# Kernel optimization log

Hardware: AMD Instinct MI355X
Metric: run time of the kernel (lower is better)

The kernel has to match this reference:

```python
import jax, jax.numpy as jnp
import numpy as np

T, B, N, H, NT = 4096, 8, 256, 512, 5
W_SCALE = 0.02


def setup_inputs() -> dict:
    key = jax.random.key(0)
    ks = jax.random.split(key, 32)
    f32 = jnp.float32
    d = {}
    d['v_action'] = jax.random.normal(ks[0], (N, B, H), f32)
    d['v_frame'] = jax.random.normal(ks[1], (T, B, H), f32)
    d['v_task'] = jax.random.normal(ks[2], (NT, B, H), f32)
    d['v_mask'] = jax.random.randint(ks[3], (B, N), 0, 2, jnp.int32).at[:, 0].set(1)
    d['t_action'] = jax.random.normal(ks[4], (N, B, H), f32)
    d['t_frame'] = jax.random.normal(ks[5], (T, B, H), f32)
    d['t_task'] = jax.random.normal(ks[6], (NT, B, H), f32)
    d['t_mask'] = jax.random.randint(ks[7], (B, N), 0, 2, jnp.int32).at[:, 0].set(1)
    names = ['v_Wq', 'v_Wk', 'v_Wv', 'v_Wo', 't_Wq', 't_Wk', 't_Wv', 't_Wo']
    for i, nm in enumerate(names):
        d[nm] = jax.random.normal(ks[8 + i], (H, H), f32) * W_SCALE
    d['v_aw'] = jnp.asarray(0.1, f32)
    d['t_aw'] = jnp.asarray(0.1, f32)
    d['v_tw'] = jax.random.normal(ks[20], (H, 1), f32) * W_SCALE
    d['v_tb'] = jnp.zeros((1,), f32)
    d['t_tw'] = jax.random.normal(ks[21], (H, 1), f32) * W_SCALE
    d['t_tb'] = jnp.zeros((1,), f32)
    return d


def _compute_logit(frame, action, Wq, Wk):
    # frame: [T,B,H] queries, action: [N,B,H] keys -> logits [B,T,N]
    q = jnp.einsum('tbf,fh->tbh', frame, Wq)
    k = jnp.einsum('nba,ah->nbh', action, Wk)
    return jnp.einsum('tbh,nbh->btn', q, k) / jnp.sqrt(jnp.asarray(q.shape[-1], q.dtype))


def _compute_output(logit, alignment, action, frame, mask, Wv, Wo, aw):
    # shared detached cross-domain alignment, gated by sigmoid(alignment_weight)
    combined = logit + jax.nn.sigmoid(aw) * alignment          # [B,T,N]
    nomask = combined
    masked = jnp.where(mask[:, None, :] > 0, combined, -jnp.inf)
    attn = jax.nn.softmax(masked, axis=-1)                      # softmax over protos N
    v = jnp.einsum('nba,af->nbf', action, Wv)                   # values from protos
    out = jnp.einsum('btn,nbf->tbf', attn, v)
    out = jnp.einsum('tbf,fg->tbg', out, Wo) + frame            # residual to frames
    return out, nomask


def reference(v_action, v_frame, v_task, v_mask, t_action, t_frame, t_task, t_mask,
              v_Wq, v_Wk, v_Wv, v_Wo, v_aw, v_tw, v_tb,
              t_Wq, t_Wk, t_Wv, t_Wo, t_aw, t_tw, t_tb):
    v_logit = _compute_logit(v_frame, v_action, v_Wq, v_Wk)
    t_logit = _compute_logit(t_frame, t_action, t_Wq, t_Wk)
    v_share = jax.lax.stop_gradient(v_logit)
    t_share = jax.lax.stop_gradient(t_logit)
    v_out, v_nm = _compute_output(v_logit, t_share, v_action, v_frame, v_mask, v_Wv, v_Wo, v_aw)
    t_out, t_nm = _compute_output(t_logit, v_share, t_action, t_frame, t_mask, t_Wv, t_Wo, t_aw)
    v_ta = jnp.einsum('kbh,ho->kbo', v_task, v_tw) + v_tb       # [ntask,B,1]
    t_ta = jnp.einsum('kbh,ho->kbo', t_task, t_tw) + t_tb
    return (v_out, t_out,
            jnp.transpose(v_nm, (0, 2, 1)),                      # [B,N,T]
            jnp.transpose(t_nm, (0, 2, 1)),
            v_ta, t_ta)
```

## Files before the change

kernel.cpp:

```cpp
#include <hip/hip_runtime.h>
#include <hip/hip_bf16.h>
#include <cstddef>
#include <cstdint>

#define T_DIM 4096
#define B_DIM 8
#define N_DIM 256
#define H_DIM 512
#define NT_DIM 5

typedef __attribute__((ext_vector_type(8))) short short8;
typedef __attribute__((ext_vector_type(4))) float f32x4;

__device__ __forceinline__ short cvt_bf16(float f) {
  __hip_bfloat16 h = __float2bfloat16(f);
  union { __hip_bfloat16 h; short s; } u; u.h = h; return u.s;
}
__device__ __forceinline__ float bf2f(short s) {
  union { uint32_t u; float f; } v; v.u = ((uint32_t)(uint16_t)s) << 16;
  return v.f;
}

typedef __attribute__((address_space(1))) const void gvoid_t;
typedef __attribute__((address_space(3))) void lvoid_t;
__device__ __forceinline__ void gl_lds16(const void* g, void* lds_wave_base) {
  __builtin_amdgcn_global_load_lds((gvoid_t*)(uintptr_t)g,
                                   (lvoid_t*)(uint32_t)(uintptr_t)lds_wave_base,
                                   16, 0, 0);
}

#define MFMA16(a, b, c) __builtin_amdgcn_mfma_f32_16x16x32_bf16(a, b, c, 0, 0, 0)

struct GP {
  const void* A[2];
  const short* B[2];
  void* C[2];
  const float* R[2];
};

template<typename TA, typename TC, bool ADD_RES>
__global__ __launch_bounds__(256)
void gemm_tn(GP p, int zlog, long long a_bs, int lda,
             long long b_bs, int ldb, long long c_bs, int ldc,
             int K, float scale) {
  constexpr bool F32A = (sizeof(TA) == 4);
  constexpr int ASTR = F32A ? 40 : 32;
  constexpr int AB = 128 * ASTR * 2;
  constexpr int BB = 128 * 32 * 2;
  constexpr int HALF = AB + BB;
  constexpr int EPIB = 4 * 16 * 68 * 4;
  constexpr int BODYB = F32A ? (2 * AB + 3 * BB) : (3 * HALF);
  constexpr int SMEMB = BODYB > EPIB ? BODYB : EPIB;
  __shared__ __align__(16) char smem[SMEMB];

  const int tid  = threadIdx.x;
  const int lane = tid & 63;
  const int wave = tid >> 6;
  const int wr   = (wave >> 1) * 64;
  const int wc   = (wave & 1) * 64;
  const int lrow = lane & 15;
  const int kgrp = lane >> 4;

  const int dom = blockIdx.z >> zlog;
  const long long zz = blockIdx.z & ((1u << zlog) - 1u);

  const TA*    Abase = (const TA*)p.A[dom] + zz * a_bs + (long long)(blockIdx.x * 128) * lda;
  const short* Bbase = p.B[dom] + zz * b_bs + (long long)(blockIdx.y * 128) * ldb;

  const int ch_r  = lane >> 2;
  const int swcol = ((lane & 3) ^ (ch_r & 3)) * 8;
  const int srow = tid >> 1;
  const int scol = (tid & 1) * 16;

  f32x4 acc[4][4] = {};
  f32x4 pv[4];

  auto stageA_bf16 = [&](int buf, int k0) {
    short* As = (short*)(smem + buf * HALF);
    #pragma unroll
    for (int i = 0; i < 2; ++i) {
      const int c = wave + 4 * i;
      gl_lds16((const short*)Abase + (long long)(c * 16 + ch_r) * lda + k0 + swcol,
               &As[c * 512]);
    }
  };
  auto stageB_bf16 = [&](int buf, int k0) {
    short* Bs = (short*)(smem + buf * HALF + AB);
    #pragma unroll
    for (int i = 0; i < 2; ++i) {
      const int c = wave + 4 * i;
      gl_lds16(Bbase + (long long)(c * 16 + ch_r) * ldb + k0 + swcol, &Bs[c * 512]);
    }
  };
  auto stageB_f32p = [&](int buf, int k0) {
    short* Bs = (short*)(smem + 2 * AB + buf * BB);
    #pragma unroll
    for (int i = 0; i < 2; ++i) {
      const int c = wave + 4 * i;
      gl_lds16(Bbase + (long long)(c * 16 + ch_r) * ldb + k0 + swcol, &Bs[c * 512]);
    }
  };
  auto loadA_f32 = [&](int k0) {
    const float* gp = (const float*)Abase + (long long)srow * lda + k0 + scol;
    pv[0] = *(const f32x4*)(gp + 0);
    pv[1] = *(const f32x4*)(gp + 4);
    pv[2] = *(const f32x4*)(gp + 8);
    pv[3] = *(const f32x4*)(gp + 12);
  };
  auto writeA_f32 = [&](int buf) {
    short* As = (short*)(smem + buf * AB);
    short8 s0, s1;
    #pragma unroll
    for (int e = 0; e < 4; ++e) {
      s0[e]     = cvt_bf16(pv[0][e]);
      s0[4 + e] = cvt_bf16(pv[1][e]);
      s1[e]     = cvt_bf16(pv[2][e]);
      s1[4 + e] = cvt_bf16(pv[3][e]);
    }
    *(short8*)&As[srow * ASTR + scol]     = s0;
    *(short8*)&As[srow * ASTR + scol + 8] = s1;
  };
  auto compute = [&](int abuf, int bbuf) {
    const short* As = (const short*)(smem + (F32A ? abuf * AB : abuf * HALF));
    const short* Bs = (const short*)(smem + (F32A ? 2 * AB + bbuf * BB
                                                  : bbuf * HALF + AB));
    short8 af[4], bfr[4];
    const int u = kgrp ^ (lrow & 3);
    #pragma unroll
    for (int i = 0; i < 4; ++i) {
      const int row = wr + i * 16 + lrow;
      if constexpr (F32A) af[i] = *(const short8*)&As[row * ASTR + kgrp * 8];
      else                af[i] = *(const short8*)&As[row * 32 + u * 8];
    }
    #pragma unroll
    for (int j = 0; j < 4; ++j) {
      const int row = wc + j * 16 + lrow;
      bfr[j] = *(const short8*)&Bs[row * 32 + u * 8];
    }
    #pragma unroll
    for (int i = 0; i < 4; ++i)
      #pragma unroll
      for (int j = 0; j < 4; ++j)
        acc[i][j] = MFMA16(af[i], bfr[j], acc[i][j]);
  };

  const int NT = K >> 5;
  if constexpr (F32A) {
    loadA_f32(0); writeA_f32(0);
    stageB_f32p(0, 0);
    if (NT > 1) stageB_f32p(1, 32);
    if (NT > 1) loadA_f32(32);
    for (int t = 0; t < NT; ++t) {
      asm volatile("s_waitcnt lgkmcnt(0)" ::: "memory");
      __builtin_amdgcn_sched_barrier(0);
      __builtin_amdgcn_s_barrier();
      if (t + 2 < NT) stageB_f32p((t + 2) % 3, (t + 2) << 5);
      __builtin_amdgcn_sched_barrier(0);
      if (t + 2 < NT)      asm volatile("s_waitcnt vmcnt(8)" ::: "memory");
      else if (t + 1 < NT) asm volatile("s_waitcnt vmcnt(6)" ::: "memory");
      else                 asm volatile("s_waitcnt vmcnt(0)" ::: "memory");
      __builtin_amdgcn_sched_barrier(0);
      __builtin_amdgcn_s_barrier();
      __builtin_amdgcn_sched_barrier(0);
      compute(t & 1, t % 3);
      if (t + 1 < NT) writeA_f32((t + 1) & 1);
      if (t + 2 < NT) loadA_f32((t + 2) << 5);
    }
  } else {
    stageA_bf16(0, 0); stageB_bf16(0, 0);
    if (NT > 1) { stageA_bf16(1, 32); stageB_bf16(1, 32); }
    for (int t = 0; t < NT; ++t) {
      __builtin_amdgcn_s_barrier();
      if (t + 2 < NT) {
        stageA_bf16((t + 2) % 3, (t + 2) << 5);
        stageB_bf16((t + 2) % 3, (t + 2) << 5);
        __builtin_amdgcn_sched_barrier(0);
        asm volatile("s_waitcnt vmcnt(8)" ::: "memory");
      } else if (t + 1 < NT) {
        asm volatile("s_waitcnt vmcnt(4)" ::: "memory");
      } else {
        asm volatile("s_waitcnt vmcnt(0)" ::: "memory");
      }
      __builtin_amdgcn_sched_barrier(0);
      __builtin_amdgcn_s_barrier();
      __builtin_amdgcn_sched_barrier(0);
      compute(t % 3, t % 3);
    }
  }

  __syncthreads();
  float* myEp = (float*)smem + wave * (16 * 68);
  TC* Cd = (TC*)p.C[dom];
  const float* Res = p.R[dom];
  const long long cb = zz * c_bs;
  const int gm = blockIdx.x * 128 + wr;
  const int gn = blockIdx.y * 128 + wc;
  const int er = lane >> 2;
  const int ec = (lane & 3) * 16;

  f32x4 resA[4], resB[4];
  if constexpr (ADD_RES) {
    const long long b0 = cb + (long long)(gm + er) * ldc + gn + ec;
    #pragma unroll
    for (int q = 0; q < 4; ++q) resA[q] = *(const f32x4*)&Res[b0 + q * 4];
  }

  #pragma unroll
  for (int i = 0; i < 4; ++i) {
    if constexpr (ADD_RES) {
      if (i < 3) {
        const long long bn = cb + (long long)(gm + (i + 1) * 16 + er) * ldc + gn + ec;
        #pragma unroll
        for (int q = 0; q < 4; ++q) resB[q] = *(const f32x4*)&Res[bn + q * 4];
      }
    }
    #pragma unroll
    for (int j = 0; j < 4; ++j)
      #pragma unroll
      for (int r = 0; r < 4; ++r)
        myEp[(kgrp * 4 + r) * 68 + j * 16 + lrow] = acc[i][j][r];
    float vals[16];
    #pragma unroll
    for (int q = 0; q < 4; ++q) {
      f32x4 t4 = *(const f32x4*)&myEp[er * 68 + ec + q * 4];
      vals[q * 4 + 0] = t4[0]; vals[q * 4 + 1] = t4[1];
      vals[q * 4 + 2] = t4[2]; vals[q * 4 + 3] = t4[3];
    }
    const int row_g = gm + i * 16 + er;
    const long long base = cb + (long long)row_g * ldc + gn + ec;
    if constexpr (sizeof(TC) == 2) {
      short8 s0, s1;
      #pragma unroll
      for (int e = 0; e < 8; ++e) {
        s0[e] = cvt_bf16(vals[e] * scale);
        s1[e] = cvt_bf16(vals[8 + e] * scale);
      }
      *(short8*)&Cd[base]     = s0;
      *(short8*)&Cd[base + 8] = s1;
    } else {
      #pragma unroll
      for (int q = 0; q < 4; ++q) {
        f32x4 o;
        #pragma unroll
        for (int e = 0; e < 4; ++e) o[e] = vals[q * 4 + e] * scale;
        if constexpr (ADD_RES) {
          #pragma unroll
          for (int e = 0; e < 4; ++e) o[e] += resA[q][e];
        }
        *(f32x4*)&Cd[base + q * 4] = o;
      }
    }
    if constexpr (ADD_RES) {
      #pragma unroll
      for (int q = 0; q < 4; ++q) resA[q] = resB[q];
    }
  }
}

struct WSrc { const float* p[8]; };

__global__ __launch_bounds__(256)
void wtrans_kernel(WSrc s, short* __restrict__ dst) {
  __shared__ float tile[32][33];
  const int w = blockIdx.z;
  const float* src = s.p[w];
  short* d = dst + (long long)w * H_DIM * H_DIM;
  const int tx = threadIdx.x, ty = threadIdx.y;
  const int n0 = blockIdx.x * 32, k0 = blockIdx.y * 32;
  #pragma unroll
  for (int i = 0; i < 4; ++i)
    tile[ty + 8 * i][tx] = src[(long long)(k0 + ty + 8 * i) * H_DIM + n0 + tx];
  __syncthreads();
  #pragma unroll
  for (int i = 0; i < 4; ++i)
    d[(long long)(n0 + ty + 8 * i) * H_DIM + k0 + tx] = cvt_bf16(tile[tx][ty + 8 * i]);
}

__global__ __launch_bounds__(256)
void softmax_fused(const short* __restrict__ Lv, const short* __restrict__ Lt,
                   const int* __restrict__ vmask, const int* __restrict__ tmask,
                   const float* __restrict__ vaw, const float* __restrict__ taw,
                   short* __restrict__ Av, short* __restrict__ At,
                   float* __restrict__ Onm_v, float* __restrict__ Onm_t) {
  __shared__ float tile[16 * 260];
  __shared__ int msk[2][256];
  const int tid = threadIdx.x;
  const int b = blockIdx.y, t0 = blockIdx.x * 16;
  const int r = tid >> 4, seg = tid & 15;
  msk[0][tid] = vmask[b * 256 + tid];
  msk[1][tid] = tmask[b * 256 + tid];
  __syncthreads();
  const float sv = 1.f / (1.f + __expf(-vaw[0]));
  const float st = 1.f / (1.f + __expf(-taw[0]));
  const long long off = ((long long)b * T_DIM + t0 + r) * N_DIM + seg * 16;

  short8 lv0 = *(const short8*)&Lv[off];
  short8 lv1 = *(const short8*)&Lv[off + 8];
  short8 lt0 = *(const short8*)&Lt[off];
  short8 lt1 = *(const short8*)&Lt[off + 8];
  float cv[16], ct[16];
  #pragma unroll
  for (int i = 0; i < 8; ++i) {
    float a0 = bf2f(lv0[i]), b0 = bf2f(lt0[i]);
    float a1 = bf2f(lv1[i]), b1 = bf2f(lt1[i]);
    cv[i]     = a0 + sv * b0;  ct[i]     = b0 + st * a0;
    cv[8 + i] = a1 + sv * b1;  ct[8 + i] = b1 + st * a1;
  }

#define EMIT_DOMAIN(CVAL, DI, AOUT, ONM) do {                                   \
    const int4 mA = *(const int4*)&msk[DI][seg * 16 + 0];                       \
    const int4 mB = *(const int4*)&msk[DI][seg * 16 + 4];                       \
    const int4 mC = *(const int4*)&msk[DI][seg * 16 + 8];                       \
    const int4 mD = *(const int4*)&msk[DI][seg * 16 + 12];                      \
    const int mk[16] = {mA.x, mA.y, mA.z, mA.w, mB.x, mB.y, mB.z, mB.w,         \
                        mC.x, mC.y, mC.z, mC.w, mD.x, mD.y, mD.z, mD.w};        \
    float mx = -3.4e38f;                                                        \
    _Pragma("unroll")                                                           \
    for (int q = 0; q < 16; ++q) if (mk[q] > 0) mx = fmaxf(mx, CVAL[q]);        \
    _Pragma("unroll")                                                           \
    for (int sh = 1; sh < 16; sh <<= 1) mx = fmaxf(mx, __shfl_xor(mx, sh));     \
    float ev[16]; float ssum = 0.f;                                             \
    _Pragma("unroll")                                                           \
    for (int q = 0; q < 16; ++q) {                                              \
      ev[q] = (mk[q] > 0) ? __expf(CVAL[q] - mx) : 0.f; ssum += ev[q];          \
    }                                                                           \
    _Pragma("unroll")                                                           \
    for (int sh = 1; sh < 16; sh <<= 1) ssum += __shfl_xor(ssum, sh);           \
    const float inv = 1.f / ssum;                                               \
    short8 o0, o1;                                                              \
    _Pragma("unroll")                                                           \
    for (int q = 0; q < 8; ++q) {                                               \
      o0[q] = cvt_bf16(ev[q] * inv); o1[q] = cvt_bf16(ev[8 + q] * inv);         \
    }                                                                           \
    *(short8*)&AOUT[off] = o0; *(short8*)&AOUT[off + 8] = o1;                   \
    _Pragma("unroll")                                                           \
    for (int q = 0; q < 4; ++q) {                                               \
      f32x4 tv; tv[0] = CVAL[q * 4]; tv[1] = CVAL[q * 4 + 1];                   \
      tv[2] = CVAL[q * 4 + 2]; tv[3] = CVAL[q * 4 + 3];                         \
      *(f32x4*)&tile[r * 260 + seg * 16 + q * 4] = tv;                          \
    }                                                                           \
    __syncthreads();                                                            \
    {                                                                           \
      float* obase = &ONM[((long long)b * N_DIM + tid) * T_DIM + t0];           \
      _Pragma("unroll")                                                         \
      for (int g = 0; g < 4; ++g) {                                             \
        f32x4 wv;                                                               \
        wv[0] = tile[(4 * g + 0) * 260 + tid];                                  \
        wv[1] = tile[(4 * g + 1) * 260 + tid];                                  \
        wv[2] = tile[(4 * g + 2) * 260 + tid];                                  \
        wv[3] = tile[(4 * g + 3) * 260 + tid];                                  \
        *(f32x4*)&obase[4 * g] = wv;                                            \
      }                                                                         \
    }                                                                           \
    __syncthreads();                                                            \
  } while (0)

  EMIT_DOMAIN(cv, 0, Av, Onm_v);
  EMIT_DOMAIN(ct, 1, At, Onm_t);
#undef EMIT_DOMAIN
}

__global__ __launch_bounds__(1024)
void task_kernel(const float* __restrict__ vtask, const float* __restrict__ ttask,
                 const float* __restrict__ vtw, const float* __restrict__ vtb,
                 const float* __restrict__ ttw, const float* __restrict__ ttb,
                 float* __restrict__ out_v, float* __restrict__ out_t) {
  const int wave = threadIdx.x >> 6;
  const int lane = threadIdx.x & 63;
  const int dom = wave >> 3;
  const int b   = wave & 7;
  const float* task = dom ? ttask : vtask;
  const float* tw   = dom ? ttw : vtw;
  const float  tb   = (dom ? ttb : vtb)[0];
  float* o = dom ? out_t : out_v;
  for (int k = 0; k < NT_DIM; ++k) {
    const float* row = task + ((long long)k * B_DIM + b) * H_DIM;
    float s = 0.f;
    for (int c = lane; c < H_DIM; c += 64) s += row[c] * tw[c];
    #pragma unroll
    for (int d = 32; d > 0; d >>= 1) s += __shfl_xor(s, d);
    if (lane == 0) o[k * B_DIM + b] = s + tb;
  }
}

extern "C" void kernel_launch(void* const* d_in, const int* in_sizes, int n_in,
                              void* d_out, int out_size, void* d_ws, size_t ws_size,
                              hipStream_t stream) {
  const float* v_action = (const float*)d_in[0];
  const float* v_frame  = (const float*)d_in[1];
  const float* v_task   = (const float*)d_in[2];
  const int*   v_mask   = (const int*)d_in[3];
  const float* t_action = (const float*)d_in[4];
  const float* t_frame  = (const float*)d_in[5];
  const float* t_task   = (const float*)d_in[6];
  const int*   t_mask   = (const int*)d_in[7];
  const float* v_aw = (const float*)d_in[16];
  const float* t_aw = (const float*)d_in[17];
  const float* v_tw = (const float*)d_in[18];
  const float* v_tb = (const float*)d_in[19];
  const float* t_tw = (const float*)d_in[20];
  const float* t_tb = (const float*)d_in[21];

  const long long TBH = (long long)T_DIM * B_DIM * H_DIM;
  const long long BTN = (long long)B_DIM * T_DIM * N_DIM;
  const long long NBH = (long long)N_DIM * B_DIM * H_DIM;
  const long long WS  = (long long)H_DIM * H_DIM;

  float* out = (float*)d_out;
  float* out_v   = out;
  float* out_t   = out + TBH;
  float* out_vnm = out + 2 * TBH;
  float* out_tnm = out + 2 * TBH + BTN;
  float* out_vta = out + 2 * TBH + 2 * BTN;
  float* out_tta = out_vta + NT_DIM * B_DIM;

  char* w = (char*)d_ws;
  auto alloc = [&](long long bytes) {
    char* p = w; w += (bytes + 255) & ~255LL; return p;
  };
  short* WT   = (short*)alloc(8 * WS * 2);
  short* Qv   = (short*)alloc(TBH * 2);
  short* Qt   = (short*)alloc(TBH * 2);
  short* KVv  = (short*)alloc(2048LL * 1024 * 2);
  short* KVt  = (short*)alloc(2048LL * 1024 * 2);
  short* VWTv = (short*)alloc(NBH * 2);
  short* VWTt = (short*)alloc(NBH * 2);
  short* Av   = (short*)alloc(BTN * 2);
  short* At   = (short*)alloc(BTN * 2);
  short* Lv   = (short*)alloc(BTN * 2);
  short* Lt   = (short*)alloc(BTN * 2);

  const float rsq = 0.044194173824159216f;

  WSrc ws8;
  for (int i = 0; i < 8; ++i) ws8.p[i] = (const float*)d_in[8 + i];
  wtrans_kernel<<<dim3(16, 16, 8), dim3(32, 8), 0, stream>>>(ws8, WT);

  {
    GP p = {{v_frame, t_frame}, {WT + 0 * WS, WT + 4 * WS}, {Qv, Qt}, {nullptr, nullptr}};
    gemm_tn<float, short, false><<<dim3(256, 4, 2), dim3(256), 0, stream>>>(
        p, 0, 0LL, H_DIM, 0LL, H_DIM, 0LL, H_DIM, 512, 1.f);
  }

  {
    GP p = {{v_action, t_action}, {WT + 1 * WS, WT + 5 * WS}, {KVv, KVt}, {nullptr, nullptr}};
    gemm_tn<float, short, false><<<dim3(16, 8, 2), dim3(256), 0, stream>>>(
        p, 0, 0LL, H_DIM, 0LL, H_DIM, 0LL, 1024, 512, 1.f);
  }

  {
    GP p = {{WT + 3 * WS, WT + 7 * WS}, {KVv + 512, KVt + 512}, {VWTv, VWTt},
            {nullptr, nullptr}};
    gemm_tn<short, short, false><<<dim3(4, 2, 16), dim3(256), 0, stream>>>(
        p, 3, 0LL, H_DIM, 1024LL, 8192, (long long)H_DIM * N_DIM, N_DIM, 512, 1.f);
  }

  {
    GP p = {{Qv, Qt}, {KVv, KVt}, {Lv, Lt}, {nullptr, nullptr}};
    gemm_tn<short, short, false><<<dim3(32, 2, 16), dim3(256), 0, stream>>>(
        p, 3, 512LL, B_DIM * H_DIM, 1024LL, 8192,
        (long long)T_DIM * N_DIM, N_DIM, 512, rsq);
  }

  softmax_fused<<<dim3(T_DIM / 16, B_DIM), dim3(256), 0, stream>>>(
      Lv, Lt, v_mask, t_mask, v_aw, t_aw, Av, At, out_vnm, out_tnm);

  {
    GP p = {{Av, At}, {VWTv, VWTt}, {out_v, out_t}, {v_frame, t_frame}};
    gemm_tn<short, float, true><<<dim3(32, 4, 16), dim3(256), 0, stream>>>(
        p, 3, (long long)T_DIM * N_DIM, N_DIM, (long long)H_DIM * N_DIM, N_DIM,
        512LL, B_DIM * H_DIM, 256, 1.f);
  }

  task_kernel<<<dim3(1), dim3(1024), 0, stream>>>(
      v_task, t_task, v_tw, v_tb, t_tw, t_tb, out_vta, out_tta);
}
```

Baseline: 290.3 us.

## Reassociate attention projections: precompute Wq·Wkᵀ and Wv·Wo, drop Q projection

Reassociates the logit computation so the frame-side Q projection (a large T×B×H by H×H GEMM) is eliminated. Instead, a combined weight M = Wq·Wkᵀ is precomputed and applied to the small action tensor, and the logit GEMM reads fp32 frames directly. Likewise Wv and Wo are fused into a single matrix applied to the actions, and the actions are converted to bf16 once. This removes a full pass over the frames plus the Q buffer write and read, at the cost of extra small weight GEMMs and a different bf16 rounding order that may change numerics.

```diff
diff --git a/kernel.cpp b/kernel.cpp
--- a/kernel.cpp
+++ b/kernel.cpp
@@ -32,10 +32,10 @@
 #define MFMA16(a, b, c) __builtin_amdgcn_mfma_f32_16x16x32_bf16(a, b, c, 0, 0, 0)
 
 struct GP {
-  const void* A[2];
-  const short* B[2];
-  void* C[2];
-  const float* R[2];
+  const void* A[4];
+  const short* B[4];
+  void* C[4];
+  const float* R[4];
 };
 
 template<typename TA, typename TC, bool ADD_RES>
@@ -257,10 +257,26 @@
   }
 }
 
-struct WSrc { const float* p[8]; };
+struct W6 { const float* p[6]; };
 
 __global__ __launch_bounds__(256)
-void wtrans_kernel(WSrc s, short* __restrict__ dst) {
+void rawcvt_kernel(W6 s, short* __restrict__ dst) {
+  const int w = blockIdx.y;
+  const float* src = s.p[w];
+  short* d = dst + (long long)w * H_DIM * H_DIM;
+  const int i = (blockIdx.x * 256 + threadIdx.x) * 8;
+  f32x4 v0 = *(const f32x4*)(src + i);
+  f32x4 v1 = *(const f32x4*)(src + i + 4);
+  short8 o;
+  #pragma unroll
+  for (int e = 0; e < 4; ++e) { o[e] = cvt_bf16(v0[e]); o[4 + e] = cvt_bf16(v1[e]); }
+  *(short8*)&d[i] = o;
+}
+
+struct W2 { const float* p[2]; };
+
+__global__ __launch_bounds__(256)
+void wtrans_kernel(W2 s, short* __restrict__ dst) {
   __shared__ float tile[32][33];
   const int w = blockIdx.z;
   const float* src = s.p[w];
@@ -274,6 +290,21 @@
   #pragma unroll
   for (int i = 0; i < 4; ++i)
     d[(long long)(n0 + ty + 8 * i) * H_DIM + k0 + tx] = cvt_bf16(tile[tx][ty + 8 * i]);
+}
+
+__global__ __launch_bounds__(256)
+void ac16_kernel(const float* __restrict__ av, const float* __restrict__ at,
+                 short* __restrict__ ov, short* __restrict__ ot) {
+  const int dom = blockIdx.y;
+  const float* src = dom ? at : av;
+  short* d = dom ? ot : ov;
+  const int i = (blockIdx.x * 256 + threadIdx.x) * 8;
+  f32x4 v0 = *(const f32x4*)(src + i);
+  f32x4 v1 = *(const f32x4*)(src + i + 4);
+  short8 o;
+  #pragma unroll
+  for (int e = 0; e < 4; ++e) { o[e] = cvt_bf16(v0[e]); o[4 + e] = cvt_bf16(v1[e]); }
+  *(short8*)&d[i] = o;
 }
 
 __global__ __launch_bounds__(256)
@@ -403,7 +434,6 @@
 
   const long long TBH = (long long)T_DIM * B_DIM * H_DIM;
   const long long BTN = (long long)B_DIM * T_DIM * N_DIM;
-  const long long NBH = (long long)N_DIM * B_DIM * H_DIM;
   const long long WS  = (long long)H_DIM * H_DIM;
 
   float* out = (float*)d_out;
@@ -418,47 +448,59 @@
   auto alloc = [&](long long bytes) {
     char* p = w; w += (bytes + 255) & ~255LL; return p;
   };
-  short* WT   = (short*)alloc(8 * WS * 2);
-  short* Qv   = (short*)alloc(TBH * 2);
-  short* Qt   = (short*)alloc(TBH * 2);
-  short* KVv  = (short*)alloc(2048LL * 1024 * 2);
-  short* KVt  = (short*)alloc(2048LL * 1024 * 2);
-  short* VWTv = (short*)alloc(NBH * 2);
-  short* VWTt = (short*)alloc(NBH * 2);
-  short* Av   = (short*)alloc(BTN * 2);
-  short* At   = (short*)alloc(BTN * 2);
-  short* Lv   = (short*)alloc(BTN * 2);
-  short* Lt   = (short*)alloc(BTN * 2);
+  short* WT    = (short*)alloc(8 * WS * 2);
+  short* Mv    = (short*)alloc(WS * 2);
+  short* Mt    = (short*)alloc(WS * 2);
+  short* PTv   = (short*)alloc(WS * 2);
+  short* PTt   = (short*)alloc(WS * 2);
+  short* Ac16v = (short*)alloc(1048576LL * 2);
+  short* Ac16t = (short*)alloc(1048576LL * 2);
+  short* KWTv  = (short*)alloc(8LL * 131072 * 2);
+  short* KWTt  = (short*)alloc(8LL * 131072 * 2);
+  short* VWTv  = (short*)alloc(8LL * 131072 * 2);
+  short* VWTt  = (short*)alloc(8LL * 131072 * 2);
+  short* Av    = (short*)alloc(BTN * 2);
+  short* At    = (short*)alloc(BTN * 2);
+  short* Lv    = (short*)alloc(BTN * 2);
+  short* Lt    = (short*)alloc(BTN * 2);
 
   const float rsq = 0.044194173824159216f;
 
-  WSrc ws8;
-  for (int i = 0; i < 8; ++i) ws8.p[i] = (const float*)d_in[8 + i];
-  wtrans_kernel<<<dim3(16, 16, 8), dim3(32, 8), 0, stream>>>(ws8, WT);
-
   {
-    GP p = {{v_frame, t_frame}, {WT + 0 * WS, WT + 4 * WS}, {Qv, Qt}, {nullptr, nullptr}};
-    gemm_tn<float, short, false><<<dim3(256, 4, 2), dim3(256), 0, stream>>>(
+    W6 s6 = {{(const float*)d_in[8], (const float*)d_in[9], (const float*)d_in[10],
+              (const float*)d_in[12], (const float*)d_in[13], (const float*)d_in[14]}};
+    rawcvt_kernel<<<dim3(128, 6), dim3(256), 0, stream>>>(s6, WT);
+    W2 s2 = {{(const float*)d_in[11], (const float*)d_in[15]}};
+    wtrans_kernel<<<dim3(16, 16, 2), dim3(32, 8), 0, stream>>>(s2, WT + 6 * WS);
+  }
+
+  ac16_kernel<<<dim3(512, 2), dim3(256), 0, stream>>>(v_action, t_action, Ac16v, Ac16t);
+
+  {
+    GP p = {{WT + 0 * WS, WT + 3 * WS, WT + 6 * WS, WT + 7 * WS},
+            {WT + 1 * WS, WT + 4 * WS, WT + 2 * WS, WT + 5 * WS},
+            {Mv, Mt, PTv, PTt},
+            {nullptr, nullptr, nullptr, nullptr}};
+    gemm_tn<short, short, false><<<dim3(4, 4, 4), dim3(256), 0, stream>>>(
         p, 0, 0LL, H_DIM, 0LL, H_DIM, 0LL, H_DIM, 512, 1.f);
   }
 
   {
-    GP p = {{v_action, t_action}, {WT + 1 * WS, WT + 5 * WS}, {KVv, KVt}, {nullptr, nullptr}};
-    gemm_tn<float, short, false><<<dim3(16, 8, 2), dim3(256), 0, stream>>>(
-        p, 0, 0LL, H_DIM, 0LL, H_DIM, 0LL, 1024, 512, 1.f);
+    GP p = {{Ac16v, Ac16t}, {Mv, Mt}, {KWTv, KWTt}, {nullptr, nullptr}};
+    gemm_tn<short, short, false><<<dim3(2, 4, 16), dim3(256), 0, stream>>>(
+        p, 3, 512LL, B_DIM * H_DIM, 0LL, H_DIM, 131072LL, H_DIM, 512, 1.f);
   }
 
   {
-    GP p = {{WT + 3 * WS, WT + 7 * WS}, {KVv + 512, KVt + 512}, {VWTv, VWTt},
-            {nullptr, nullptr}};
+    GP p = {{PTv, PTt}, {Ac16v, Ac16t}, {VWTv, VWTt}, {nullptr, nullptr}};
     gemm_tn<short, short, false><<<dim3(4, 2, 16), dim3(256), 0, stream>>>(
-        p, 3, 0LL, H_DIM, 1024LL, 8192, (long long)H_DIM * N_DIM, N_DIM, 512, 1.f);
+        p, 3, 0LL, H_DIM, 512LL, B_DIM * H_DIM, 131072LL, N_DIM, 512, 1.f);
   }
 
   {
-    GP p = {{Qv, Qt}, {KVv, KVt}, {Lv, Lt}, {nullptr, nullptr}};
-    gemm_tn<short, short, false><<<dim3(32, 2, 16), dim3(256), 0, stream>>>(
-        p, 3, 512LL, B_DIM * H_DIM, 1024LL, 8192,
+    GP p = {{v_frame, t_frame}, {KWTv, KWTt}, {Lv, Lt}, {nullptr, nullptr}};
+    gemm_tn<float, short, false><<<dim3(32, 2, 16), dim3(256), 0, stream>>>(
+        p, 3, 512LL, B_DIM * H_DIM, 131072LL, H_DIM,
         (long long)T_DIM * N_DIM, N_DIM, 512, rsq);
   }
 
@@ -468,7 +510,7 @@
   {
     GP p = {{Av, At}, {VWTv, VWTt}, {out_v, out_t}, {v_frame, t_frame}};
     gemm_tn<short, float, true><<<dim3(32, 4, 16), dim3(256), 0, stream>>>(
-        p, 3, (long long)T_DIM * N_DIM, N_DIM, (long long)H_DIM * N_DIM, N_DIM,
+        p, 3, (long long)T_DIM * N_DIM, N_DIM, 131072LL, N_DIM,
         512LL, B_DIM * H_DIM, 256, 1.f);
   }
 
```

Result: faster. 246.0 us (-15.3%).
